# Performance work log

Measured on AMD Instinct MI355X. Metric: run time of the kernel, lower is better.

Reference implementation:

```python
import jax, jax.numpy as jnp
import numpy as np

B, NQ, S, D = 8, 1024, 2048, 512

def setup_inputs() -> dict:
    key = jax.random.key(0)
    k1, k2, k3, k4 = jax.random.split(key, 4)
    queries = jax.random.normal(k1, (B, NQ, D), dtype=jnp.float32)
    keys = jax.random.normal(k2, (B, S, D), dtype=jnp.float32)
    values = jax.random.normal(k3, (B, S, D), dtype=jnp.float32)
    mask = jax.random.randint(k4, (B, NQ, S), 0, 2, dtype=jnp.int32)
    return {"queries": queries, "keys": keys, "values": values, "mask": mask}

def reference(queries, keys, values, mask):
    # scores: dot-product attention scores (b, nq, s)
    scores = jnp.einsum('bqd,bsd->bqs', queries, keys)
    attention_dist = jax.nn.softmax(scores, axis=2)
    # mask then renormalize over seq axis
    attention_dist = attention_dist * mask.astype(attention_dist.dtype)
    attention_dist = attention_dist / attention_dist.sum(axis=2, keepdims=True)
    # weighted sum of values: equivalent to (dist.unsqueeze(3) * values.unsqueeze(1)).sum(2)
    final_vector = jnp.einsum('bqs,bsd->bqd', attention_dist, values)
    return final_vector
```

## Files before the change

### kernel.cpp

```cpp
#include <hip/hip_runtime.h>


#define Bz 8
#define NQz 1024
#define Sz 2048
#define Dz 512
#define QTT 128
#define TS 32
#define KP 520
#define PP 40

typedef _Float16 f16x8 __attribute__((ext_vector_type(8)));
typedef float f32x4 __attribute__((ext_vector_type(4)));
typedef unsigned short ushort_t;

#define AS1(p) ((const __attribute__((address_space(1))) unsigned int*)(p))
#define AS3(p) ((__attribute__((address_space(3))) unsigned int*)(p))
#define DRAIN_ALL() __builtin_amdgcn_s_waitcnt(0)

__device__ __forceinline__ ushort_t f2h(float x) {
  _Float16 h = (_Float16)x;
  return __builtin_bit_cast(ushort_t, h);
}
__device__ __forceinline__ float h2f(ushort_t u) {
  return (float)__builtin_bit_cast(_Float16, u);
}

__global__ __launch_bounds__(256)
void prep(const float* __restrict__ K, const float* __restrict__ V,
          const int* __restrict__ Mi, ushort_t* __restrict__ Kf,
          ushort_t* __restrict__ Vt, unsigned* __restrict__ Mp) {
  __shared__ ushort_t sT[64][41];
  const int t = threadIdx.x;
  int bx = blockIdx.x;
  if (bx < 2048) {
    const size_t base = (size_t)bx * 4096 + t * 4;
#pragma unroll
    for (int i = 0; i < 4; ++i) {
      size_t e = base + i * 1024;
      float4 v = *(const float4*)(K + e);
      uint2 w;
      w.x = (unsigned)f2h(v.x) | ((unsigned)f2h(v.y) << 16);
      w.y = (unsigned)f2h(v.z) | ((unsigned)f2h(v.w) << 16);
      *(uint2*)(Kf + e) = w;
    }
    return;
  }
  bx -= 2048;
  if (bx < 4096) {
    const int b = bx >> 9;
    const int rest = bx & 511;
    const int st = rest >> 4;
    const int dt = rest & 15;
    const int s0 = st * 64, d0 = dt * 32;
    const float* Vb = V + ((size_t)b * Sz + s0) * Dz + d0;
#pragma unroll
    for (int i = 0; i < 2; ++i) {
      int idx = t + 256 * i;
      int s = idx >> 3;
      int dc = (idx & 7) * 4;
      float4 v = *(const float4*)(Vb + (size_t)s * Dz + dc);
      uint2 w;
      w.x = (unsigned)f2h(v.x) | ((unsigned)f2h(v.y) << 16);
      w.y = (unsigned)f2h(v.z) | ((unsigned)f2h(v.w) << 16);
      *(uint2*)(&sT[s][dc]) = w;
    }
    __syncthreads();
    ushort_t* VtB = Vt + ((size_t)b * Dz + d0) * Sz + s0;
    int d = t >> 3, c = t & 7;
    uint4 u;
    ushort_t* tp = (ushort_t*)&u;
#pragma unroll
    for (int j = 0; j < 8; ++j) tp[j] = sT[c * 8 + j][d];
    *(uint4*)(VtB + (size_t)d * Sz + c * 8) = u;
    return;
  }
  bx -= 4096;
  const int lane = t & 63;
#pragma unroll
  for (int i = 0; i < 4; ++i) {
    const size_t base = (size_t)bx * 4096 + i * 1024 + t * 4;
    const int4 mv = *(const int4*)(Mi + base);
    unsigned nib = (mv.x ? 1u : 0u) | (mv.y ? 2u : 0u) |
                   (mv.z ? 4u : 0u) | (mv.w ? 8u : 0u);
    unsigned v = nib << ((lane & 7) * 4);
    v |= __shfl_xor(v, 1);
    v |= __shfl_xor(v, 2);
    v |= __shfl_xor(v, 4);
    if ((lane & 7) == 0) Mp[bx * 128 + i * 32 + (t >> 3)] = v;
  }
}

template <int SPLIT>
__global__ __launch_bounds__(512, 2)
void attn_flash(const float* __restrict__ Q, const unsigned* __restrict__ Mp,
                const ushort_t* __restrict__ Kf, const ushort_t* __restrict__ Vt,
                ushort_t* __restrict__ Opart, float* __restrict__ Mpart,
                float* __restrict__ Lpart) {
  __shared__ ushort_t sK[2][TS][KP];
  __shared__ ushort_t sV[2][Dz][TS];
  __shared__ ushort_t sP[8][16][PP];

  const int tid  = threadIdx.x;
  const int wave = tid >> 6;
  const int lane = tid & 63;
  const int l16  = lane & 15;
  const int quad = lane >> 4;

  const int bxr = blockIdx.x;
  const int b   = bxr & 7;
  const int rest = bxr >> 3;
  const int qt  = rest / SPLIT;
  const int sh  = rest % SPLIT;
  const int q0  = qt * QTT;
  const int SLEN = Sz / SPLIT;
  const int NTt  = SLEN / TS;
  const int sbeg = sh * SLEN;
  const int qw   = q0 + wave * 16;

  const float*    Qb  = Q  + ((size_t)b * NQz + qw) * Dz;
  const ushort_t* KfB = Kf + (size_t)b * Sz * Dz;
  const ushort_t* VtB = Vt + (size_t)b * Dz * Sz;
  const unsigned* MpB = Mp + ((size_t)b * NQz + qw) * (Sz / 32);

  const int vql  = (lane & 3) ^ ((lane >> 3) & 3);
  const int vcol = (quad ^ ((l16 >> 1) & 3)) * 8;

  auto issue_tile = [&](int s0n, int bsel) {
#pragma unroll
    for (int j = 0; j < 4; ++j) {
      int row = wave * 4 + j;
      const ushort_t* gp = KfB + (size_t)(s0n + row) * Dz + lane * 8;
      __builtin_amdgcn_global_load_lds(AS1(gp), AS3(&sK[bsel][row][0]), 16, 0, 0);
    }
#pragma unroll
    for (int j = 0; j < 4; ++j) {
      int dbase = wave * 64 + j * 16;
      int d = dbase + (lane >> 2);
      const ushort_t* gp = VtB + (size_t)d * Sz + s0n + vql * 8;
      __builtin_amdgcn_global_load_lds(AS1(gp), AS3(&sV[bsel][dbase][0]), 16, 0, 0);
    }
  };
  auto load_mask = [&](int s0n) -> unsigned {
    return MpB[(size_t)l16 * (Sz / 32) + (s0n >> 5)];
  };

  issue_tile(sbeg, 0);
  unsigned msk_cur = load_mask(sbeg);

  f16x8 qa[16];
  {
    const float* qrow = Qb + (size_t)l16 * Dz;
#pragma unroll
    for (int kk = 0; kk < 16; ++kk) {
      const float4 a = *(const float4*)(qrow + kk * 32 + quad * 8);
      const float4 c = *(const float4*)(qrow + kk * 32 + quad * 8 + 4);
      f16x8 h;
      h[0] = (_Float16)a.x; h[1] = (_Float16)a.y;
      h[2] = (_Float16)a.z; h[3] = (_Float16)a.w;
      h[4] = (_Float16)c.x; h[5] = (_Float16)c.y;
      h[6] = (_Float16)c.z; h[7] = (_Float16)c.w;
      qa[kk] = h;
    }
  }
  if (NTt > 1) issue_tile(sbeg + TS, 1);
  DRAIN_ALL();
  __syncthreads();

  float m_ln = -1e30f, l_ln = 0.0f;
  f32x4 oacc[32];
#pragma unroll
  for (int nt = 0; nt < 32; ++nt) oacc[nt] = (f32x4){0.f, 0.f, 0.f, 0.f};

  const ushort_t* vbase0 = &sV[0][0][0] + (size_t)l16 * TS + vcol;
  const ushort_t* vbase1 = &sV[1][0][0] + (size_t)l16 * TS + vcol;

  for (int i = 0; i < NTt; ++i) {
    const int buf = i & 1;
    if (i) {
      DRAIN_ALL();
      __syncthreads();
      if (i + 1 < NTt) issue_tile(sbeg + (i + 1) * TS, buf ^ 1);
    }
    unsigned msk_nxt = (i + 1 < NTt) ? load_mask(sbeg + (i + 1) * TS) : 0u;

    f32x4 a00 = (f32x4){0.f,0.f,0.f,0.f}, a01 = (f32x4){0.f,0.f,0.f,0.f};
    f32x4 a10 = (f32x4){0.f,0.f,0.f,0.f}, a11 = (f32x4){0.f,0.f,0.f,0.f};
    {
      const ushort_t* kh0 = &sK[buf][l16][quad * 8];
      const ushort_t* kh1 = &sK[buf][16 + l16][quad * 8];
#pragma unroll
      for (int kk = 0; kk < 16; kk += 2) {
        f16x8 k00 = *(const f16x8*)(kh0 + kk * 32);
        f16x8 k10 = *(const f16x8*)(kh1 + kk * 32);
        f16x8 k01 = *(const f16x8*)(kh0 + kk * 32 + 32);
        f16x8 k11 = *(const f16x8*)(kh1 + kk * 32 + 32);
        a00 = __builtin_amdgcn_mfma_f32_16x16x32_f16(k00, qa[kk], a00, 0, 0, 0);
        a10 = __builtin_amdgcn_mfma_f32_16x16x32_f16(k10, qa[kk], a10, 0, 0, 0);
        a01 = __builtin_amdgcn_mfma_f32_16x16x32_f16(k01, qa[kk+1], a01, 0, 0, 0);
        a11 = __builtin_amdgcn_mfma_f32_16x16x32_f16(k11, qa[kk+1], a11, 0, 0, 0);
      }
    }
    f32x4 s0v, s1v;
#pragma unroll
    for (int r = 0; r < 4; ++r) { s0v[r] = a00[r] + a01[r]; s1v[r] = a10[r] + a11[r]; }

    const unsigned mb = msk_cur;
    float se0[4], se1[4];
#pragma unroll
    for (int r = 0; r < 4; ++r) {
      se0[r] = ((mb >> (quad * 4 + r)) & 1u)      ? s0v[r] : -1e30f;
      se1[r] = ((mb >> (16 + quad * 4 + r)) & 1u) ? s1v[r] : -1e30f;
    }
    float rmax = fmaxf(fmaxf(fmaxf(se0[0], se0[1]), fmaxf(se0[2], se0[3])),
                       fmaxf(fmaxf(se1[0], se1[1]), fmaxf(se1[2], se1[3])));
    rmax = fmaxf(rmax, __shfl_xor(rmax, 16));
    rmax = fmaxf(rmax, __shfl_xor(rmax, 32));

    ushort_t pb0[4], pb1[4];
    float rsum = 0.f;
#pragma unroll
    for (int r = 0; r < 4; ++r) {
      float p0 = ((mb >> (quad * 4 + r)) & 1u)      ? __expf(se0[r] - rmax) : 0.f;
      float p1 = ((mb >> (16 + quad * 4 + r)) & 1u) ? __expf(se1[r] - rmax) : 0.f;
      pb0[r] = f2h(p0); pb1[r] = f2h(p1);
      rsum += p0 + p1;
    }
    {
      uint2 w0, w1;
      w0.x = (unsigned)pb0[0] | ((unsigned)pb0[1] << 16);
      w0.y = (unsigned)pb0[2] | ((unsigned)pb0[3] << 16);
      w1.x = (unsigned)pb1[0] | ((unsigned)pb1[1] << 16);
      w1.y = (unsigned)pb1[2] | ((unsigned)pb1[3] << 16);
      *(uint2*)(&sP[wave][l16][quad * 4]) = w0;
      *(uint2*)(&sP[wave][l16][16 + quad * 4]) = w1;
    }
    rsum += __shfl_xor(rsum, 16);
    rsum += __shfl_xor(rsum, 32);

    float m_new = fmaxf(m_ln, rmax);
    float scl   = __expf(rmax - m_new);
    float al_ln = __expf(m_ln - m_new);
    bool  grw   = m_new > m_ln;
    l_ln = al_ln * l_ln + scl * rsum;
    m_ln = m_new;

    f16x8 praw = *(const f16x8*)(&sP[wave][l16][quad * 8]);
    f16x8 pa;
    {
      _Float16 sh16 = (_Float16)scl;
#pragma unroll
      for (int j = 0; j < 8; ++j) pa[j] = praw[j] * sh16;
    }

    if (__any((int)grw)) {
      float al[4];
#pragma unroll
      for (int r = 0; r < 4; ++r) al[r] = __shfl(al_ln, quad * 4 + r);
#pragma unroll
      for (int nt = 0; nt < 32; ++nt)
#pragma unroll
        for (int r = 0; r < 4; ++r) oacc[nt][r] *= al[r];
    }

    const ushort_t* vb_ = buf ? vbase1 : vbase0;
#pragma unroll
    for (int nt = 0; nt < 32; ++nt) {
      f16x8 vb = *(const f16x8*)(vb_ + nt * 512);
      oacc[nt] = __builtin_amdgcn_mfma_f32_16x16x32_f16(pa, vb, oacc[nt], 0, 0, 0);
    }

    msk_cur = msk_nxt;
  }

  const size_t rbase = (size_t)(b * SPLIT + sh) * NQz + q0 + wave * 16;
#pragma unroll
  for (int nt = 0; nt < 32; ++nt) {
#pragma unroll
    for (int r = 0; r < 4; ++r) {
      Opart[(rbase + quad * 4 + r) * Dz + nt * 16 + l16] = f2h(oacc[nt][r]);
    }
  }
  if (quad == 0) {
    Mpart[rbase + l16] = m_ln;
    Lpart[rbase + l16] = l_ln;
  }
}

template <int SPLIT>
__global__ __launch_bounds__(256)
void combine(const ushort_t* __restrict__ Opart, const float* __restrict__ Mpart,
             const float* __restrict__ Lpart, float* __restrict__ Out) {
  int gid = blockIdx.x * 256 + threadIdx.x;
  int row = gid >> 7;
  int b   = row >> 10;
  int q   = row & 1023;
  int c   = (gid & 127) * 4;
  float mv[SPLIT], lv[SPLIT];
  float m = -1e30f;
#pragma unroll
  for (int p = 0; p < SPLIT; ++p) {
    size_t ip = (size_t)(b * SPLIT + p) * NQz + q;
    mv[p] = Mpart[ip];
    lv[p] = Lpart[ip];
    m = fmaxf(m, mv[p]);
  }
  float w[SPLIT], denom = 0.f;
#pragma unroll
  for (int p = 0; p < SPLIT; ++p) {
    w[p] = __expf(mv[p] - m);
    denom += w[p] * lv[p];
  }
  float inv = 1.0f / denom;
  float4 o = {0.f, 0.f, 0.f, 0.f};
#pragma unroll
  for (int p = 0; p < SPLIT; ++p) {
    size_t ip = (size_t)(b * SPLIT + p) * NQz + q;
    const ushort_t* op = Opart + ip * Dz + c;
    uint2 raw = *(const uint2*)op;
    o.x += w[p] * h2f((ushort_t)(raw.x & 0xffff));
    o.y += w[p] * h2f((ushort_t)(raw.x >> 16));
    o.z += w[p] * h2f((ushort_t)(raw.y & 0xffff));
    o.w += w[p] * h2f((ushort_t)(raw.y >> 16));
  }
  o.x *= inv; o.y *= inv; o.z *= inv; o.w *= inv;
  *(float4*)(Out + ((size_t)b * NQz + q) * Dz + c) = o;
}

extern "C" void kernel_launch(void* const* d_in, const int* in_sizes, int n_in,
                              void* d_out, int out_size, void* d_ws, size_t ws_size,
                              hipStream_t stream) {
  const float* Q = (const float*)d_in[0];
  const float* K = (const float*)d_in[1];
  const float* V = (const float*)d_in[2];
  const int*   M = (const int*)d_in[3];
  float* O = (float*)d_out;

  const size_t NKV   = (size_t)Bz * Sz * Dz;
  const size_t maskW = (size_t)Bz * NQz * (Sz / 32);

  ushort_t* Kf = (ushort_t*)d_ws;
  ushort_t* Vt = Kf + NKV;
  unsigned* Mp = (unsigned*)(Vt + NKV);
  ushort_t* Opart = (ushort_t*)(Mp + maskW);

  auto need_bytes = [&](int S) -> size_t {
    return NKV * 2 * 2 + maskW * 4
         + (size_t)Bz * S * NQz * Dz * 2
         + (size_t)Bz * S * NQz * 4 * 2;
  };

  prep<<<dim3(10240), dim3(256), 0, stream>>>(K, V, M, Kf, Vt, Mp);

  if (ws_size >= need_bytes(4)) {
    constexpr int S = 4;
    float* Mpart = (float*)(Opart + (size_t)Bz * S * NQz * Dz);
    float* Lpart = Mpart + (size_t)Bz * S * NQz;
    attn_flash<S><<<dim3(8 * (NQz / QTT) * S), dim3(512), 0, stream>>>(
        Q, Mp, Kf, Vt, Opart, Mpart, Lpart);
    combine<S><<<dim3(4096), dim3(256), 0, stream>>>(Opart, Mpart, Lpart, O);
  } else {
    constexpr int S = 2;
    float* Mpart = (float*)(Opart + (size_t)Bz * S * NQz * Dz);
    float* Lpart = Mpart + (size_t)Bz * S * NQz;
    attn_flash<S><<<dim3(8 * (NQz / QTT) * S), dim3(512), 0, stream>>>(
        Q, Mp, Kf, Vt, Opart, Mpart, Lpart);
    combine<S><<<dim3(4096), dim3(256), 0, stream>>>(Opart, Mpart, Lpart, O);
  }
}
```

Baseline: 246.5 us.

## Read V directly from global memory and shrink query tile to 64

Removes the shared-memory staging of the transposed V tile. Each wave now loads its V fragments directly from global memory (via cache) in batches of eight before the PV MFMAs. The query tile is halved to 64 rows with 256-thread blocks, so the grid doubles and LDS use per block drops, which may raise occupancy. In exchange, V is re-read from global/L2 by every wave and by twice as many blocks, and these loads are not overlapped by the double-buffered async pipeline.

```diff
diff --git a/kernel.cpp b/kernel.cpp
--- a/kernel.cpp
+++ b/kernel.cpp
@@ -5,7 +5,7 @@
 #define NQz 1024
 #define Sz 2048
 #define Dz 512
-#define QTT 128
+#define QTT 64
 #define TS 32
 #define KP 520
 #define PP 40
@@ -92,14 +92,13 @@
 }
 
 template <int SPLIT>
-__global__ __launch_bounds__(512, 2)
+__global__ __launch_bounds__(256, 2)
 void attn_flash(const float* __restrict__ Q, const unsigned* __restrict__ Mp,
                 const ushort_t* __restrict__ Kf, const ushort_t* __restrict__ Vt,
                 ushort_t* __restrict__ Opart, float* __restrict__ Mpart,
                 float* __restrict__ Lpart) {
   __shared__ ushort_t sK[2][TS][KP];
-  __shared__ ushort_t sV[2][Dz][TS];
-  __shared__ ushort_t sP[8][16][PP];
+  __shared__ ushort_t sP[4][16][PP];
 
   const int tid  = threadIdx.x;
   const int wave = tid >> 6;
@@ -123,29 +122,19 @@
   const ushort_t* VtB = Vt + (size_t)b * Dz * Sz;
   const unsigned* MpB = Mp + ((size_t)b * NQz + qw) * (Sz / 32);
 
-  const int vql  = (lane & 3) ^ ((lane >> 3) & 3);
-  const int vcol = (quad ^ ((l16 >> 1) & 3)) * 8;
-
-  auto issue_tile = [&](int s0n, int bsel) {
-#pragma unroll
-    for (int j = 0; j < 4; ++j) {
-      int row = wave * 4 + j;
+  auto issue_k = [&](int s0n, int bsel) {
+#pragma unroll
+    for (int j = 0; j < 8; ++j) {
+      int row = wave * 8 + j;
       const ushort_t* gp = KfB + (size_t)(s0n + row) * Dz + lane * 8;
       __builtin_amdgcn_global_load_lds(AS1(gp), AS3(&sK[bsel][row][0]), 16, 0, 0);
-    }
-#pragma unroll
-    for (int j = 0; j < 4; ++j) {
-      int dbase = wave * 64 + j * 16;
-      int d = dbase + (lane >> 2);
-      const ushort_t* gp = VtB + (size_t)d * Sz + s0n + vql * 8;
-      __builtin_amdgcn_global_load_lds(AS1(gp), AS3(&sV[bsel][dbase][0]), 16, 0, 0);
     }
   };
   auto load_mask = [&](int s0n) -> unsigned {
     return MpB[(size_t)l16 * (Sz / 32) + (s0n >> 5)];
   };
 
-  issue_tile(sbeg, 0);
+  issue_k(sbeg, 0);
   unsigned msk_cur = load_mask(sbeg);
 
   f16x8 qa[16];
@@ -163,7 +152,7 @@
       qa[kk] = h;
     }
   }
-  if (NTt > 1) issue_tile(sbeg + TS, 1);
+  if (NTt > 1) issue_k(sbeg + TS, 1);
   DRAIN_ALL();
   __syncthreads();
 
@@ -172,17 +161,15 @@
 #pragma unroll
   for (int nt = 0; nt < 32; ++nt) oacc[nt] = (f32x4){0.f, 0.f, 0.f, 0.f};
 
-  const ushort_t* vbase0 = &sV[0][0][0] + (size_t)l16 * TS + vcol;
-  const ushort_t* vbase1 = &sV[1][0][0] + (size_t)l16 * TS + vcol;
-
   for (int i = 0; i < NTt; ++i) {
     const int buf = i & 1;
+    const int s0  = sbeg + i * TS;
     if (i) {
       DRAIN_ALL();
       __syncthreads();
-      if (i + 1 < NTt) issue_tile(sbeg + (i + 1) * TS, buf ^ 1);
-    }
-    unsigned msk_nxt = (i + 1 < NTt) ? load_mask(sbeg + (i + 1) * TS) : 0u;
+      if (i + 1 < NTt) issue_k(s0 + TS, buf ^ 1);
+    }
+    unsigned msk_nxt = (i + 1 < NTt) ? load_mask(s0 + TS) : 0u;
 
     f32x4 a00 = (f32x4){0.f,0.f,0.f,0.f}, a01 = (f32x4){0.f,0.f,0.f,0.f};
     f32x4 a10 = (f32x4){0.f,0.f,0.f,0.f}, a11 = (f32x4){0.f,0.f,0.f,0.f};
@@ -263,11 +250,19 @@
         for (int r = 0; r < 4; ++r) oacc[nt][r] *= al[r];
     }
 
-    const ushort_t* vb_ = buf ? vbase1 : vbase0;
-#pragma unroll
-    for (int nt = 0; nt < 32; ++nt) {
-      f16x8 vb = *(const f16x8*)(vb_ + nt * 512);
-      oacc[nt] = __builtin_amdgcn_mfma_f32_16x16x32_f16(pa, vb, oacc[nt], 0, 0, 0);
+    {
+      const ushort_t* VtL = VtB + (size_t)l16 * Sz + s0 + quad * 8;
+#pragma unroll
+      for (int c = 0; c < 4; ++c) {
+        f16x8 vb[8];
+#pragma unroll
+        for (int j = 0; j < 8; ++j)
+          vb[j] = *(const f16x8*)(VtL + (size_t)((c * 8 + j) * 16) * Sz);
+#pragma unroll
+        for (int j = 0; j < 8; ++j)
+          oacc[c * 8 + j] = __builtin_amdgcn_mfma_f32_16x16x32_f16(
+              pa, vb[j], oacc[c * 8 + j], 0, 0, 0);
+      }
     }
 
     msk_cur = msk_nxt;
@@ -356,14 +351,14 @@
     constexpr int S = 4;
     float* Mpart = (float*)(Opart + (size_t)Bz * S * NQz * Dz);
     float* Lpart = Mpart + (size_t)Bz * S * NQz;
-    attn_flash<S><<<dim3(8 * (NQz / QTT) * S), dim3(512), 0, stream>>>(
+    attn_flash<S><<<dim3(8 * (NQz / QTT) * S), dim3(256), 0, stream>>>(
         Q, Mp, Kf, Vt, Opart, Mpart, Lpart);
     combine<S><<<dim3(4096), dim3(256), 0, stream>>>(Opart, Mpart, Lpart, O);
   } else {
     constexpr int S = 2;
     float* Mpart = (float*)(Opart + (size_t)Bz * S * NQz * Dz);
     float* Lpart = Mpart + (size_t)Bz * S * NQz;
-    attn_flash<S><<<dim3(8 * (NQz / QTT) * S), dim3(512), 0, stream>>>(
+    attn_flash<S><<<dim3(8 * (NQz / QTT) * S), dim3(256), 0, stream>>>(
         Q, Mp, Kf, Vt, Opart, Mpart, Lpart);
     combine<S><<<dim3(4096), dim3(256), 0, stream>>>(Opart, Mpart, Lpart, O);
   }
```

Result: slower. 318.9 us (+29.4%).
